# Performance work log

Hardware: AMD Instinct MI355X
Metric: run time of the kernel (lower is better)

Reference implementation:

```python
import jax, jax.numpy as jnp
import numpy as np

KH = KW = 3  # kernel spatial size is hard-coded to 3 in the original layer


def _tdiv2(x):
    # matches tf.cast(x / 2, tf.int32): true-divide by 2, truncate toward zero
    return jnp.trunc(x * 0.5)


def setup_inputs() -> dict:
    key = jax.random.key(0)
    k1, k2, k3 = jax.random.split(key, 3)
    B, H, W, C, F = 4, 32, 32, 64, 128
    # integer-valued tensors stored as float32 (bit-serial math needs integer weights)
    inputs = jax.random.randint(k1, (B, H, W, C), 0, 16).astype(jnp.float32)
    kernel = jax.random.randint(k2, (KH, KW, C, F), -8, 8).astype(jnp.float32)
    bias = jax.random.randint(k3, (F,), -4, 4).astype(jnp.float32)
    return {"inputs": inputs, "kernel": kernel, "bias": bias, "bits": 4}


def reference(inputs, kernel, bias, bits):
    # Bit-serial conv2d, padding='same' (pad=1), activation='relu'.
    # Per (kernel position, input element, output channel) the original computes
    #   acc <- trunc((acc + x * (w mod 2) * sign(w_orig)) / 2); w <- trunc(w / 2)
    # for `bits` iterations, then sums over channels/kernel window.
    B, H, W, C = inputs.shape
    F = kernel.shape[-1]
    x = jnp.pad(inputs, ((0, 0), (1, 1), (1, 1), (0, 0)))  # 'same' padding, pad=1
    out = jnp.zeros((B, H, W, F), inputs.dtype)
    for i in range(KH):
        for j in range(KW):
            patch = x[:, i:i + H, j:j + W, :][..., None]   # [B,H,W,C,1]
            w = kernel[i, j]                               # [C,F]
            s = jnp.sign(w)                                # sign of ORIGINAL weight, fixed
            acc = jnp.zeros((B, H, W, C, F), inputs.dtype)
            ww = w
            for _ in range(bits):
                acc = _tdiv2(acc + patch * (jnp.mod(ww, 2.0) * s))
                ww = _tdiv2(ww)
            out = out + acc.sum(axis=3)                    # sum over C; kernel window summed by loop
    return jax.nn.relu(out + bias)
```

## Files before the change

kernel.cpp:

```cpp
#include <hip/hip_runtime.h>
#include <stdint.h>


#define XOFF 36864
#define NXPK 147968

static __device__ __forceinline__ int pk_mad_i16(int a, int b, int c) {
    int d;
    asm("v_pk_mad_i16 %0, %1, %2, %3" : "=v"(d) : "v"(a), "v"(b), "v"(c));
    return d;
}
static __device__ __forceinline__ int pk_ashr(int sh, int a) {
    int d;
    asm("v_pk_ashrrev_i16 %0, %1, %2" : "=v"(d) : "v"(sh), "v"(a));
    return d;
}
static __device__ __forceinline__ int pk_add_i16(int a, int b) {
    int d;
    asm("v_pk_add_i16 %0, %1, %2" : "=v"(d) : "v"(a), "v"(b));
    return d;
}

__global__ __launch_bounds__(256) void prep_all(const float* __restrict__ kern,
                                                const float* __restrict__ input,
                                                uint32_t* __restrict__ ws) {
    int bid = blockIdx.x, tid = threadIdx.x;
    if (bid < 144) {
        int t    = bid * 256 + tid;
        int u    = t & 3;
        int rest = t >> 2;
        int f64  = rest & 63;
        int ce   = (rest >> 6) & 7;
        int kifh = rest >> 9;
        int fh   = kifh & 1;
        int ki   = kifh >> 1;
        int c    = ce * 8 + u * 2;
        int f    = fh * 64 + f64;
        int wlo = (int)kern[(ki * 64 + c    ) * 128 + f];
        int whi = (int)kern[(ki * 64 + c + 1) * 128 + f];
        ws[t] = (uint32_t)(uint16_t)(int16_t)wlo |
                ((uint32_t)(uint16_t)(int16_t)whi << 16);
    } else {
        int t = (bid - 144) * 256 + tid;
        if (t >= NXPK) return;
        int c2    = t & 31;
        int rest  = t >> 5;
        int wp    = rest % 34;
        int rest2 = rest / 34;
        int hp    = rest2 % 34;
        int b     = rest2 / 34;
        int v = 0;
        if (hp >= 1 && hp <= 32 && wp >= 1 && wp <= 32) {
            const float* p = &input[(((b * 32) + hp - 1) * 32 + (wp - 1)) * 64 + c2 * 2];
            v = (int)p[0] | ((int)p[1] << 16);
        }
        ws[XOFF + t] = (uint32_t)v;
    }
}

__global__ __launch_bounds__(512, 4) void conv_main(const uint32_t* __restrict__ ws,
                                                    const float* __restrict__ bias,
                                                    float* __restrict__ out) {
    const uint32_t* xpk = ws + XOFF;

    int bid = blockIdx.x;
    int fh  = bid & 1;
    int wq  = (bid >> 1) & 7;
    int h   = (bid >> 4) & 31;
    int b   = bid >> 9;
    int tid = threadIdx.x;
    int f64 = tid & 63;
    int ce  = tid >> 6;
    int w0  = wq * 4;

    __shared__ uint32_t xl[3 * 6 * 32];
    __shared__ int prt[8 * 4 * 64];

    #pragma unroll
    for (int pass = 0; pass < 2; ++pass) {
        int k = pass * 512 + tid;
        if (k < 576) {
            int c2  = k & 31;
            int rc  = k >> 5;
            int col = rc % 6;
            int r   = rc / 6;
            xl[k] = xpk[((b * 34 + h + r) * 34 + (w0 + col)) * 32 + c2];
        }
    }

    int4 wv[9];
    const int4* wp4 = (const int4*)ws;
    #pragma unroll
    for (int ki = 0; ki < 9; ++ki) wv[ki] = wp4[(ki * 2 + fh) * 512 + tid];

    __syncthreads();

    const int SH4  = 0x00040004;
    const int SH15 = 0x000F000F;
    int acc0 = 0, acc1 = 0, acc2 = 0, acc3 = 0;

    #pragma unroll
    for (int row = 0; row < 3; ++row) {
        const uint32_t* xb = xl + (row * 6) * 32 + ce * 4;
        int4 xc[6];
        #pragma unroll
        for (int cidx = 0; cidx < 6; ++cidx)
            xc[cidx] = *(const int4*)(xb + cidx * 32);
        #pragma unroll
        for (int j = 0; j < 3; ++j) {
            const int4 w4 = wv[row * 3 + j];
            #pragma unroll
            for (int u = 0; u < 4; ++u) {
                int w2 = (&w4.x)[u];
                int A  = pk_ashr(SH15, w2) & 0x000F000F;
                acc0 = pk_add_i16(acc0, pk_ashr(SH4, pk_mad_i16((&xc[j + 0].x)[u], w2, A)));
                acc1 = pk_add_i16(acc1, pk_ashr(SH4, pk_mad_i16((&xc[j + 1].x)[u], w2, A)));
                acc2 = pk_add_i16(acc2, pk_ashr(SH4, pk_mad_i16((&xc[j + 2].x)[u], w2, A)));
                acc3 = pk_add_i16(acc3, pk_ashr(SH4, pk_mad_i16((&xc[j + 3].x)[u], w2, A)));
            }
        }
    }

    prt[(ce * 4 + 0) * 64 + f64] = (int)(short)(acc0 & 0xffff) + (acc0 >> 16);
    prt[(ce * 4 + 1) * 64 + f64] = (int)(short)(acc1 & 0xffff) + (acc1 >> 16);
    prt[(ce * 4 + 2) * 64 + f64] = (int)(short)(acc2 & 0xffff) + (acc2 >> 16);
    prt[(ce * 4 + 3) * 64 + f64] = (int)(short)(acc3 & 0xffff) + (acc3 >> 16);
    __syncthreads();

    if (tid < 256) {
        int ff = tid & 63;
        int px = tid >> 6;
        int v = 0;
        #pragma unroll
        for (int e = 0; e < 8; ++e) v += prt[(e * 4 + px) * 64 + ff];
        v += (int)bias[fh * 64 + ff];
        out[((b * 32 + h) * 32 + w0 + px) * 128 + fh * 64 + ff] =
            (float)(v < 0 ? 0 : v);
    }
}

extern "C" void kernel_launch(void* const* d_in, const int* in_sizes, int n_in,
                              void* d_out, int out_size, void* d_ws, size_t ws_size,
                              hipStream_t stream) {
    const float* input  = (const float*)d_in[0];
    const float* kernel = (const float*)d_in[1];
    const float* bias   = (const float*)d_in[2];

    uint32_t* ws = (uint32_t*)d_ws;

    prep_all<<<144 + 579, 256, 0, stream>>>(kernel, input, ws);
    conv_main<<<2048, 512, 0, stream>>>(ws, bias, (float*)d_out);
}
```

Measured before the change: 79.67 us.

## Fuse input/weight packing into conv kernel and accumulate with dot2

Removes the separate prep kernel that packed weights and padded inputs into a workspace; the conv kernel now reads float inputs and weights directly, packs them to int16 pairs on the fly, and handles padding with bounds checks into a reshaped shared tile. The packed i16 adds are replaced with v_dot2_i32_i16 against ones, so accumulation is in 32-bit and the final lane merge is dropped. This saves a launch and a workspace round trip, at the cost of every block redundantly converting weights from strided float loads.

```diff
diff --git a/kernel.cpp b/kernel.cpp
--- a/kernel.cpp
+++ b/kernel.cpp
@@ -1,9 +1,6 @@
 #include <hip/hip_runtime.h>
 #include <stdint.h>
 
-
-#define XOFF 36864
-#define NXPK 147968
 
 static __device__ __forceinline__ int pk_mad_i16(int a, int b, int c) {
     int d;
@@ -15,54 +12,14 @@
     asm("v_pk_ashrrev_i16 %0, %1, %2" : "=v"(d) : "v"(sh), "v"(a));
     return d;
 }
-static __device__ __forceinline__ int pk_add_i16(int a, int b) {
-    int d;
-    asm("v_pk_add_i16 %0, %1, %2" : "=v"(d) : "v"(a), "v"(b));
-    return d;
+static __device__ __forceinline__ void dot2_acc(int& acc, int t, int ones) {
+    asm("v_dot2_i32_i16 %0, %1, %2, %0" : "+v"(acc) : "v"(t), "v"(ones));
 }
 
-__global__ __launch_bounds__(256) void prep_all(const float* __restrict__ kern,
-                                                const float* __restrict__ input,
-                                                uint32_t* __restrict__ ws) {
-    int bid = blockIdx.x, tid = threadIdx.x;
-    if (bid < 144) {
-        int t    = bid * 256 + tid;
-        int u    = t & 3;
-        int rest = t >> 2;
-        int f64  = rest & 63;
-        int ce   = (rest >> 6) & 7;
-        int kifh = rest >> 9;
-        int fh   = kifh & 1;
-        int ki   = kifh >> 1;
-        int c    = ce * 8 + u * 2;
-        int f    = fh * 64 + f64;
-        int wlo = (int)kern[(ki * 64 + c    ) * 128 + f];
-        int whi = (int)kern[(ki * 64 + c + 1) * 128 + f];
-        ws[t] = (uint32_t)(uint16_t)(int16_t)wlo |
-                ((uint32_t)(uint16_t)(int16_t)whi << 16);
-    } else {
-        int t = (bid - 144) * 256 + tid;
-        if (t >= NXPK) return;
-        int c2    = t & 31;
-        int rest  = t >> 5;
-        int wp    = rest % 34;
-        int rest2 = rest / 34;
-        int hp    = rest2 % 34;
-        int b     = rest2 / 34;
-        int v = 0;
-        if (hp >= 1 && hp <= 32 && wp >= 1 && wp <= 32) {
-            const float* p = &input[(((b * 32) + hp - 1) * 32 + (wp - 1)) * 64 + c2 * 2];
-            v = (int)p[0] | ((int)p[1] << 16);
-        }
-        ws[XOFF + t] = (uint32_t)v;
-    }
-}
-
-__global__ __launch_bounds__(512, 4) void conv_main(const uint32_t* __restrict__ ws,
-                                                    const float* __restrict__ bias,
-                                                    float* __restrict__ out) {
-    const uint32_t* xpk = ws + XOFF;
-
+__global__ __launch_bounds__(512, 4) void conv_fused(const float* __restrict__ input,
+                                                     const float* __restrict__ kern,
+                                                     const float* __restrict__ bias,
+                                                     float* __restrict__ out) {
     int bid = blockIdx.x;
     int fh  = bid & 1;
     int wq  = (bid >> 1) & 7;
@@ -73,35 +30,52 @@
     int ce  = tid >> 6;
     int w0  = wq * 4;
 
-    __shared__ uint32_t xl[3 * 6 * 32];
+    __shared__ uint32_t xl[3 * 8 * 32];
     __shared__ int prt[8 * 4 * 64];
 
     #pragma unroll
     for (int pass = 0; pass < 2; ++pass) {
         int k = pass * 512 + tid;
-        if (k < 576) {
+        if (pass == 0 || k < 768) {
             int c2  = k & 31;
-            int rc  = k >> 5;
-            int col = rc % 6;
-            int r   = rc / 6;
-            xl[k] = xpk[((b * 34 + h + r) * 34 + (w0 + col)) * 32 + c2];
+            int col = (k >> 5) & 7;
+            int r   = k >> 8;
+            int gh  = h + r - 1;
+            int gw  = w0 + col - 1;
+            uint32_t v = 0;
+            if ((unsigned)gh < 32u && (unsigned)gw < 32u && col < 6) {
+                const float* p = &input[(((b * 32) + gh) * 32 + gw) * 64 + c2 * 2];
+                v = (uint32_t)((int)p[0] | ((int)p[1] << 16));
+            }
+            xl[k] = v;
         }
     }
 
     int4 wv[9];
-    const int4* wp4 = (const int4*)ws;
-    #pragma unroll
-    for (int ki = 0; ki < 9; ++ki) wv[ki] = wp4[(ki * 2 + fh) * 512 + tid];
+    {
+        const float* kp = kern + ce * 1024 + fh * 64 + f64;
+        #pragma unroll
+        for (int ki = 0; ki < 9; ++ki) {
+            const float* kpi = kp + ki * 8192;
+            #pragma unroll
+            for (int u = 0; u < 4; ++u) {
+                int lo = (int)kpi[(u * 2    ) * 128];
+                int hi = (int)kpi[(u * 2 + 1) * 128];
+                (&wv[ki].x)[u] = (lo & 0xffff) | (hi << 16);
+            }
+        }
+    }
 
     __syncthreads();
 
     const int SH4  = 0x00040004;
     const int SH15 = 0x000F000F;
+    const int ONES = 0x00010001;
     int acc0 = 0, acc1 = 0, acc2 = 0, acc3 = 0;
 
     #pragma unroll
     for (int row = 0; row < 3; ++row) {
-        const uint32_t* xb = xl + (row * 6) * 32 + ce * 4;
+        const uint32_t* xb = xl + row * 256 + ce * 4;
         int4 xc[6];
         #pragma unroll
         for (int cidx = 0; cidx < 6; ++cidx)
@@ -113,18 +87,18 @@
             for (int u = 0; u < 4; ++u) {
                 int w2 = (&w4.x)[u];
                 int A  = pk_ashr(SH15, w2) & 0x000F000F;
-                acc0 = pk_add_i16(acc0, pk_ashr(SH4, pk_mad_i16((&xc[j + 0].x)[u], w2, A)));
-                acc1 = pk_add_i16(acc1, pk_ashr(SH4, pk_mad_i16((&xc[j + 1].x)[u], w2, A)));
-                acc2 = pk_add_i16(acc2, pk_ashr(SH4, pk_mad_i16((&xc[j + 2].x)[u], w2, A)));
-                acc3 = pk_add_i16(acc3, pk_ashr(SH4, pk_mad_i16((&xc[j + 3].x)[u], w2, A)));
+                dot2_acc(acc0, pk_ashr(SH4, pk_mad_i16((&xc[j + 0].x)[u], w2, A)), ONES);
+                dot2_acc(acc1, pk_ashr(SH4, pk_mad_i16((&xc[j + 1].x)[u], w2, A)), ONES);
+                dot2_acc(acc2, pk_ashr(SH4, pk_mad_i16((&xc[j + 2].x)[u], w2, A)), ONES);
+                dot2_acc(acc3, pk_ashr(SH4, pk_mad_i16((&xc[j + 3].x)[u], w2, A)), ONES);
             }
         }
     }
 
-    prt[(ce * 4 + 0) * 64 + f64] = (int)(short)(acc0 & 0xffff) + (acc0 >> 16);
-    prt[(ce * 4 + 1) * 64 + f64] = (int)(short)(acc1 & 0xffff) + (acc1 >> 16);
-    prt[(ce * 4 + 2) * 64 + f64] = (int)(short)(acc2 & 0xffff) + (acc2 >> 16);
-    prt[(ce * 4 + 3) * 64 + f64] = (int)(short)(acc3 & 0xffff) + (acc3 >> 16);
+    prt[(ce * 4 + 0) * 64 + f64] = acc0;
+    prt[(ce * 4 + 1) * 64 + f64] = acc1;
+    prt[(ce * 4 + 2) * 64 + f64] = acc2;
+    prt[(ce * 4 + 3) * 64 + f64] = acc3;
     __syncthreads();
 
     if (tid < 256) {
@@ -146,8 +120,5 @@
     const float* kernel = (const float*)d_in[1];
     const float* bias   = (const float*)d_in[2];
 
-    uint32_t* ws = (uint32_t*)d_ws;
-
-    prep_all<<<144 + 579, 256, 0, stream>>>(kernel, input, ws);
-    conv_main<<<2048, 512, 0, stream>>>(ws, bias, (float*)d_out);
+    conv_fused<<<2048, 512, 0, stream>>>(input, kernel, bias, (float*)d_out);
 }
```

After: 83.57 us. 1.05x slower.
